# Kernel tuning notes

Hardware: AMD Instinct MI355X
Metric: run time of the kernel (lower is better)

Reference implementation:

```python
import jax, jax.numpy as jnp
import numpy as np

B, IN, HID, OUT = 1024, 512, 128, 64
INP1 = IN + 1  # 513, after prepending ones column


def setup_inputs() -> dict:
    key = jax.random.key(0)
    k1, k2, k3, k4, k5, k6, k7, k8 = jax.random.split(key, 8)
    s1 = 1.0 / np.sqrt(INP1 * INP1)
    s2 = 1.0 / np.sqrt(HID)
    return {
        "img": jax.random.normal(k1, (B, IN), dtype=jnp.float32),
        "tab": jax.random.normal(k2, (B, IN), dtype=jnp.float32),
        "W1": jax.random.uniform(k3, (HID, INP1 * INP1), jnp.float32, -s1, s1),
        "b1": jax.random.uniform(k4, (HID,), jnp.float32, -s1, s1),
        "W2": jax.random.uniform(k5, (HID, HID), jnp.float32, -s2, s2),
        "b2": jax.random.uniform(k6, (HID,), jnp.float32, -s2, s2),
        "W3": jax.random.uniform(k7, (OUT, HID), jnp.float32, -s2, s2),
        "b3": jax.random.uniform(k8, (OUT,), jnp.float32, -s2, s2),
    }


def reference(img, tab, W1, b1, W2, b2, W3, b3):
    ones = jnp.ones((img.shape[0], 1), dtype=img.dtype)
    x = jnp.concatenate([ones, img], axis=1)  # [B, IN+1]
    t = jnp.concatenate([ones, tab], axis=1)  # [B, IN+1]
    # batched outer product, flattened: [B, (IN+1)*(IN+1)]
    fusion = jnp.einsum("bi,bj->bij", x, t).reshape(x.shape[0], -1)
    # dropout is identity in eval mode
    y1 = fusion @ W1.T + b1
    y2 = jnp.tanh(y1 @ W2.T + b2)
    y3 = jax.nn.relu(y2 @ W3.T + b3)
    return y3
```

## Files before the change

kernel.cpp:

```cpp
#include <hip/hip_runtime.h>
#include <hip/hip_bf16.h>

typedef __bf16 bf16x8 __attribute__((ext_vector_type(8)));
typedef float f32x4 __attribute__((ext_vector_type(4)));
typedef float f32x4u __attribute__((ext_vector_type(4), aligned(4)));
typedef unsigned short u16x8 __attribute__((ext_vector_type(8)));

typedef __attribute__((address_space(1))) const unsigned int gu32;
typedef __attribute__((address_space(3))) unsigned int lu32;

#define B_SZ   1024
#define IN_SZ  512
#define HID    128
#define OUT_SZ 64
#define BK     32
#define NKT    16
#define M2     65536

static __device__ __forceinline__ unsigned short f2bf(float f) {
    __hip_bfloat16 h = __float2bfloat16(f);
    return *reinterpret_cast<unsigned short*>(&h);
}

__global__ __launch_bounds__(256) void prep_kernel(
    const float* __restrict__ img, const float* __restrict__ tab,
    const float* __restrict__ w1,
    unsigned short* __restrict__ tbt, float* __restrict__ xhT,
    float* __restrict__ tc, float* __restrict__ wrowT,
    unsigned short* __restrict__ w1c)
{
    const int blk = blockIdx.x;
    {
        const size_t e = ((size_t)blk * 256 + threadIdx.x) * 8;
        const int r  = (int)(e >> 9);
        const int c8 = (int)(e & 511);
        const size_t srow = (size_t)(r >> 9) * 513 + (r & 511);
        const float* src = w1 + srow * 513 + c8;
        const f32x4u lo = *reinterpret_cast<const f32x4u*>(src);
        const f32x4u hi = *reinterpret_cast<const f32x4u*>(src + 4);
        u16x8 u;
        u[0] = f2bf(lo[0]); u[1] = f2bf(lo[1]); u[2] = f2bf(lo[2]); u[3] = f2bf(lo[3]);
        u[4] = f2bf(hi[0]); u[5] = f2bf(hi[1]); u[6] = f2bf(hi[2]); u[7] = f2bf(hi[3]);
        *reinterpret_cast<u16x8*>(w1c + (size_t)r * 512 + c8) = u;
    }
    if (blk < 1024) {
        for (int j = threadIdx.x; j < 512; j += 256) {
            float v = (j == 0) ? 1.0f : tab[(size_t)blk * IN_SZ + (j - 1)];
            tbt[(size_t)blk * 512 + j] = f2bf(v);
        }
        if (threadIdx.x == 0) tc[blk] = tab[(size_t)blk * IN_SZ + 511];
    }
    if (blk < 513) {
        for (int b = threadIdx.x; b < B_SZ; b += 256)
            xhT[(size_t)blk * B_SZ + b] =
                (blk == 0) ? 1.0f : img[(size_t)b * IN_SZ + (blk - 1)];
    }
    if (blk < 257) {
        const int idx = blk * 256 + threadIdx.x;
        if (idx < 513 * 128) {
            const int j = idx >> 7, h = idx & 127;
            wrowT[idx] = w1[((size_t)h * 513 + 512) * 513 + j];
        }
    }
}

__global__ __launch_bounds__(256, 3) void gemm_fused(
    const float* __restrict__ w1, const unsigned short* __restrict__ w1c,
    const unsigned short* __restrict__ tbt,
    const float* __restrict__ xhT, const float* __restrict__ tc,
    float* __restrict__ y1acc)
{
    __shared__ unsigned short Als[3][128 * BK];
    __shared__ unsigned short Bls[3][128 * BK];

    const int wgid = (blockIdx.x & 7) * 512 + (blockIdx.x >> 3);
    const int bm = wgid >> 3;
    const int bn = wgid & 7;
    const int m0 = bm * 128;
    const int n0 = bn * 128;
    const int h0    = bm >> 2;
    const int ibase = (bm & 3) * 128;
    const int tid  = threadIdx.x;
    const int wv   = tid >> 6;
    const int wr   = wv >> 1;
    const int wc   = wv & 1;
    const int lane = tid & 63;
    const int l15  = lane & 15;
    const int kg   = lane >> 4;

    const unsigned short* asrc[2];
    const unsigned short* bsrc[2];
    int sBase[2];
    #pragma unroll
    for (int q = 0; q < 2; ++q) {
        const int p  = q * 256 + tid;
        const int r  = p >> 2;
        const int cl = (p & 3) ^ ((r >> 1) & 3);
        asrc[q] = w1c + (size_t)(m0 + r) * 512 + cl * 8;
        bsrc[q] = tbt + (size_t)(n0 + r) * 512 + cl * 8;
        sBase[q] = (q * 256 + wv * 64) * 8;
    }

    int aoffs[4], boffs[4];
    #pragma unroll
    for (int ms = 0; ms < 4; ++ms) {
        const int r = wr * 64 + ms * 16 + l15;
        aoffs[ms] = (r * 4 + (kg ^ ((r >> 1) & 3))) * 8;
    }
    #pragma unroll
    for (int ns = 0; ns < 4; ++ns) {
        const int r = wc * 64 + ns * 16 + l15;
        boffs[ns] = (r * 4 + (kg ^ ((r >> 1) & 3))) * 8;
    }

    f32x4 acc[4][4] = {};

#define STG(BUF, KT) do {                                                    \
        const int k32_ = (KT) * BK;                                          \
        _Pragma("unroll")                                                    \
        for (int q_ = 0; q_ < 2; ++q_) {                                     \
            __builtin_amdgcn_global_load_lds(                                \
                (gu32*)(const void*)(asrc[q_] + k32_),                       \
                (lu32*)(void*)&Als[BUF][sBase[q_]], 16, 0, 0);               \
            __builtin_amdgcn_global_load_lds(                                \
                (gu32*)(const void*)(bsrc[q_] + k32_),                       \
                (lu32*)(void*)&Bls[BUF][sBase[q_]], 16, 0, 0);               \
        }                                                                    \
    } while (0)

    STG(0, 0);
    STG(1, 1);

    #pragma unroll
    for (int kt = 0; kt < NKT; ++kt) {
        if (kt == NKT - 1) asm volatile("s_waitcnt vmcnt(0)" ::: "memory");
        else               asm volatile("s_waitcnt vmcnt(4)" ::: "memory");
        __builtin_amdgcn_s_barrier();
        __builtin_amdgcn_sched_barrier(0);

        if (kt + 2 < NKT) STG((kt + 2) % 3, kt + 2);

        const int cur = kt % 3;
        const unsigned short* ab = &Als[cur][0];
        const unsigned short* bb = &Bls[cur][0];
        bf16x8 af[4], bfr[4];
        #pragma unroll
        for (int ms = 0; ms < 4; ++ms)
            af[ms] = *reinterpret_cast<const bf16x8*>(&ab[aoffs[ms]]);
        #pragma unroll
        for (int ns = 0; ns < 4; ++ns)
            bfr[ns] = *reinterpret_cast<const bf16x8*>(&bb[boffs[ns]]);
        __builtin_amdgcn_s_setprio(1);
        #pragma unroll
        for (int ms = 0; ms < 4; ++ms)
            #pragma unroll
            for (int ns = 0; ns < 4; ++ns)
                acc[ms][ns] = __builtin_amdgcn_mfma_f32_16x16x32_bf16(
                    af[ms], bfr[ns], acc[ms][ns], 0, 0, 0);
        __builtin_amdgcn_s_setprio(0);
    }
#undef STG

    const size_t orow = (size_t)h0 * 513;
    float wcv[4][4];
    #pragma unroll
    for (int ms = 0; ms < 4; ++ms)
        #pragma unroll
        for (int v = 0; v < 4; ++v) {
            const int i_ = ibase + wr * 64 + ms * 16 + kg * 4 + v;
            wcv[ms][v] = w1[(orow + i_) * 513 + 512];
        }

    #pragma unroll
    for (int ns = 0; ns < 4; ++ns) {
        const int ncol = n0 + wc * 64 + ns * 16 + l15;
        const float tv = tc[ncol];
        float s0 = 0.f;
        #pragma unroll
        for (int ms = 0; ms < 4; ++ms) {
            const int i_ = ibase + wr * 64 + ms * 16 + kg * 4;
            #pragma unroll
            for (int v = 0; v < 4; ++v)
                s0 += (acc[ms][ns][v] + wcv[ms][v] * tv)
                      * xhT[(size_t)(i_ + v) * B_SZ + ncol];
        }
        s0 += __shfl_xor(s0, 16); s0 += __shfl_xor(s0, 32);
        if (lane < 16) atomicAdd(&y1acc[(size_t)ncol * HID + h0], s0);
    }
}

__global__ __launch_bounds__(128) void tailmlp_kernel(
    const float* __restrict__ img, const float* __restrict__ tab,
    const float* __restrict__ wrowT, const float* __restrict__ y1acc,
    const float* __restrict__ b1,
    const float* __restrict__ W2, const float* __restrict__ b2,
    const float* __restrict__ W3, const float* __restrict__ b3,
    float* __restrict__ out)
{
    __shared__ float tls[4][513];
    __shared__ float W2p[128][129];
    __shared__ float W3p[64][129];
    __shared__ float y1ls[4][128];
    __shared__ float y2ls[4][128];

    const int b0 = blockIdx.x * 4;
    const int h  = threadIdx.x;

    #pragma unroll
    for (int g = 0; g < 128; ++g) {
        const int idx = g * 128 + h;
        W2p[idx >> 7][idx & 127] = W2[idx];
    }
    #pragma unroll
    for (int g = 0; g < 64; ++g) {
        const int idx = g * 128 + h;
        W3p[idx >> 7][idx & 127] = W3[idx];
    }
    #pragma unroll
    for (int q = 0; q < 4; ++q)
        for (int j = h; j < 513; j += 128)
            tls[q][j] = (j == 0) ? 1.0f : tab[(size_t)(b0 + q) * IN_SZ + (j - 1)];
    __syncthreads();

    {
        float a0 = 0.f, a1 = 0.f, a2 = 0.f, a3 = 0.f;
        #pragma unroll 8
        for (int j = 0; j < 513; ++j) {
            const float w = wrowT[j * 128 + h];
            a0 += w * tls[0][j]; a1 += w * tls[1][j];
            a2 += w * tls[2][j]; a3 += w * tls[3][j];
        }
        const float bb = b1[h];
        y1ls[0][h] = y1acc[(size_t)(b0 + 0) * HID + h] + bb
                     + a0 * img[(size_t)(b0 + 0) * IN_SZ + 511];
        y1ls[1][h] = y1acc[(size_t)(b0 + 1) * HID + h] + bb
                     + a1 * img[(size_t)(b0 + 1) * IN_SZ + 511];
        y1ls[2][h] = y1acc[(size_t)(b0 + 2) * HID + h] + bb
                     + a2 * img[(size_t)(b0 + 2) * IN_SZ + 511];
        y1ls[3][h] = y1acc[(size_t)(b0 + 3) * HID + h] + bb
                     + a3 * img[(size_t)(b0 + 3) * IN_SZ + 511];
    }
    __syncthreads();

    {
        const float bb = b2[h];
        float s[4] = {bb, bb, bb, bb};
        #pragma unroll 16
        for (int k = 0; k < HID; ++k) {
            const float w = W2p[h][k];
            s[0] += w * y1ls[0][k]; s[1] += w * y1ls[1][k];
            s[2] += w * y1ls[2][k]; s[3] += w * y1ls[3][k];
        }
        #pragma unroll
        for (int q = 0; q < 4; ++q) y2ls[q][h] = tanhf(s[q]);
    }
    __syncthreads();

    if (h < OUT_SZ) {
        const float bb = b3[h];
        float s[4] = {bb, bb, bb, bb};
        #pragma unroll 16
        for (int k = 0; k < HID; ++k) {
            const float w = W3p[h][k];
            s[0] += w * y2ls[0][k]; s[1] += w * y2ls[1][k];
            s[2] += w * y2ls[2][k]; s[3] += w * y2ls[3][k];
        }
        #pragma unroll
        for (int q = 0; q < 4; ++q)
            out[(size_t)(b0 + q) * OUT_SZ + h] = fmaxf(s[q], 0.f);
    }
}

__global__ __launch_bounds__(512, 4) void gemm_fused_fb(
    const float* __restrict__ w1, const unsigned short* __restrict__ tbt,
    const float* __restrict__ xhT, const float* __restrict__ tc,
    float* __restrict__ y1acc)
{
    __shared__ float          Afs[2][64 * BK];
    __shared__ unsigned short Bls[2][512 * BK];

    const int bm = blockIdx.x >> 1;
    const int bn = blockIdx.x & 1;
    const int m0 = bm * 64;
    const int n0 = bn * 512;
    const int tid  = threadIdx.x;
    const int wv   = tid >> 6;
    const int lane = tid & 63;
    const int l15  = lane & 15;
    const int kg   = lane >> 4;

    const int ar  = tid >> 3;
    const int acl = (tid & 7) ^ (ar & 7);
    const float* asrc = w1 + (size_t)(m0 + ar) * 513 + acl * 4;
    const int aBase = (wv * 64) * 4;

    const unsigned short* bsrc[4];
    int bBase[4];
    #pragma unroll
    for (int q = 0; q < 4; ++q) {
        const int p  = q * 512 + tid;
        const int r  = p >> 2;
        const int cl = (p & 3) ^ ((r >> 1) & 3);
        bsrc[q] = tbt + (size_t)(n0 + r) * 512 + cl * 8;
        bBase[q] = (q * 512 + wv * 64) * 8;
    }

    int aoff0[4], aoff1[4], boffs[4];
    #pragma unroll
    for (int ms = 0; ms < 4; ++ms) {
        const int r = ms * 16 + l15;
        aoff0[ms] = r * 32 + (((kg * 2) + 0) ^ (r & 7)) * 4;
        aoff1[ms] = r * 32 + (((kg * 2) + 1) ^ (r & 7)) * 4;
    }
    #pragma unroll
    for (int ns = 0; ns < 4; ++ns) {
        const int r = wv * 64 + ns * 16 + l15;
        boffs[ns] = ((r << 2) | (kg ^ ((r >> 1) & 3))) * 8;
    }

    f32x4 acc[4][4] = {};

#define STAGE_FB(BUF, KT) do {                                               \
        const int k32_ = (KT) * BK;                                          \
        _Pragma("unroll")                                                    \
        for (int q_ = 0; q_ < 4; ++q_)                                       \
            __builtin_amdgcn_global_load_lds(                                \
                (gu32*)(const void*)(bsrc[q_] + k32_),                       \
                (lu32*)(void*)&Bls[BUF][bBase[q_]], 16, 0, 0);               \
        __builtin_amdgcn_global_load_lds(                                    \
            (gu32*)(const void*)(asrc + k32_),                               \
            (lu32*)(void*)&Afs[BUF][aBase], 16, 0, 0);                       \
    } while (0)

    STAGE_FB(0, 0);
    __syncthreads();

    for (int kt = 0; kt < NKT; ++kt) {
        const int cur = kt & 1;
        if (kt + 1 < NKT) STAGE_FB(cur ^ 1, kt + 1);

        const float*          ab = &Afs[cur][0];
        const unsigned short* bb = &Bls[cur][0];
        bf16x8 bfr[4];
        #pragma unroll
        for (int ns = 0; ns < 4; ++ns)
            bfr[ns] = *reinterpret_cast<const bf16x8*>(&bb[boffs[ns]]);
        #pragma unroll
        for (int ms = 0; ms < 4; ++ms) {
            const f32x4 lo = *reinterpret_cast<const f32x4*>(&ab[aoff0[ms]]);
            const f32x4 hi = *reinterpret_cast<const f32x4*>(&ab[aoff1[ms]]);
            u16x8 u;
            u[0] = f2bf(lo[0]); u[1] = f2bf(lo[1]);
            u[2] = f2bf(lo[2]); u[3] = f2bf(lo[3]);
            u[4] = f2bf(hi[0]); u[5] = f2bf(hi[1]);
            u[6] = f2bf(hi[2]); u[7] = f2bf(hi[3]);
            const bf16x8 af = __builtin_bit_cast(bf16x8, u);
            #pragma unroll
            for (int ns = 0; ns < 4; ++ns)
                acc[ms][ns] = __builtin_amdgcn_mfma_f32_16x16x32_bf16(
                    af, bfr[ns], acc[ms][ns], 0, 0, 0);
        }
        __syncthreads();
    }
#undef STAGE_FB

    const int h0 = m0 / 513;
    const int mb = (h0 + 1) * 513;
    const bool cross = (mb < m0 + 64);

    float wcv[4][4];
    #pragma unroll
    for (int ms = 0; ms < 4; ++ms)
        #pragma unroll
        for (int v = 0; v < 4; ++v)
            wcv[ms][v] = w1[(size_t)(m0 + ms * 16 + kg * 4 + v) * 513 + 512];

    #pragma unroll
    for (int ns = 0; ns < 4; ++ns) {
        const int ncol = n0 + wv * 64 + ns * 16 + l15;
        const float tv = tc[ncol];
        float s0 = 0.f, s1 = 0.f;
        #pragma unroll
        for (int ms = 0; ms < 4; ++ms) {
            #pragma unroll
            for (int v = 0; v < 4; ++v) {
                const int m = m0 + ms * 16 + kg * 4 + v;
                const bool lo = (m < mb);
                const int i = lo ? (m - h0 * 513) : (m - mb);
                const float val = (acc[ms][ns][v] + wcv[ms][v] * tv)
                                  * xhT[(size_t)i * B_SZ + ncol];
                if (lo) s0 += val; else s1 += val;
            }
        }
        s0 += __shfl_xor(s0, 16); s0 += __shfl_xor(s0, 32);
        if (lane < 16) atomicAdd(&y1acc[(size_t)ncol * HID + h0], s0);
        if (cross) {
            s1 += __shfl_xor(s1, 16); s1 += __shfl_xor(s1, 32);
            if (lane < 16 && (h0 + 1) < HID)
                atomicAdd(&y1acc[(size_t)ncol * HID + h0 + 1], s1);
        }
    }
}

__global__ __launch_bounds__(256) void prep_fb_kernel(
    const float* __restrict__ img, const float* __restrict__ tab,
    unsigned short* __restrict__ tbt, float* __restrict__ xhT,
    float* __restrict__ tc)
{
    const int blk = blockIdx.x;
    for (int j = threadIdx.x; j < 512; j += 256) {
        float v = (j == 0) ? 1.0f : tab[(size_t)blk * IN_SZ + (j - 1)];
        tbt[(size_t)blk * 512 + j] = f2bf(v);
    }
    if (threadIdx.x == 0) tc[blk] = tab[(size_t)blk * IN_SZ + 511];
    if (blk < 513) {
        for (int b = threadIdx.x; b < B_SZ; b += 256)
            xhT[(size_t)blk * B_SZ + b] =
                (blk == 0) ? 1.0f : img[(size_t)b * IN_SZ + (blk - 1)];
    }
}

__global__ __launch_bounds__(128) void mlp_kernel(
    const float* __restrict__ y1acc, const float* __restrict__ b1,
    const float* __restrict__ W2, const float* __restrict__ b2,
    const float* __restrict__ W3, const float* __restrict__ b3,
    float* __restrict__ out)
{
    __shared__ float y1r[HID];
    __shared__ float y2r[HID];
    const int b = blockIdx.x;
    const int h = threadIdx.x;
    y1r[h] = y1acc[(size_t)b * HID + h] + b1[h];
    __syncthreads();
    float a = b2[h];
    const float* w2r = W2 + (size_t)h * HID;
    #pragma unroll 8
    for (int k = 0; k < HID; ++k) a += w2r[k] * y1r[k];
    y2r[h] = tanhf(a);
    __syncthreads();
    if (h < OUT_SZ) {
        float a3 = b3[h];
        const float* w3r = W3 + (size_t)h * HID;
        #pragma unroll 8
        for (int k = 0; k < HID; ++k) a3 += w3r[k] * y2r[k];
        out[(size_t)b * OUT_SZ + h] = fmaxf(a3, 0.f);
    }
}

extern "C" void kernel_launch(void* const* d_in, const int* in_sizes, int n_in,
                              void* d_out, int out_size, void* d_ws, size_t ws_size,
                              hipStream_t stream) {
    const float* img = (const float*)d_in[0];
    const float* tab = (const float*)d_in[1];
    const float* W1  = (const float*)d_in[2];
    const float* b1  = (const float*)d_in[3];
    const float* W2  = (const float*)d_in[4];
    const float* b2  = (const float*)d_in[5];
    const float* W3  = (const float*)d_in[6];
    const float* b3  = (const float*)d_in[7];
    float* out = (float*)d_out;

    char* ws = (char*)d_ws;
    float*          y1acc = (float*)ws;
    unsigned short* tbt   = (unsigned short*)(ws + 524288);
    float*          xhT   = (float*)(ws + 1572864);
    float*          tc    = (float*)(ws + 3674112);
    float*          wrowT = (float*)(ws + 3678208);
    unsigned short* w1c   = (unsigned short*)(ws + 3940864);
    const size_t need = 3940864ULL + 67108864ULL;

    hipMemsetAsync(y1acc, 0, (size_t)B_SZ * HID * sizeof(float), stream);
    if (ws_size >= need) {
        prep_kernel<<<dim3(16384), dim3(256), 0, stream>>>(
            img, tab, W1, tbt, xhT, tc, wrowT, w1c);
        gemm_fused<<<dim3(4096), dim3(256), 0, stream>>>(
            W1, w1c, tbt, xhT, tc, y1acc);
        tailmlp_kernel<<<dim3(256), dim3(128), 0, stream>>>(
            img, tab, wrowT, y1acc, b1, W2, b2, W3, b3, out);
    } else {
        prep_fb_kernel<<<dim3(1024), dim3(256), 0, stream>>>(img, tab, tbt, xhT, tc);
        gemm_fused_fb<<<dim3(2052), dim3(512), 0, stream>>>(W1, tbt, xhT, tc, y1acc);
        mlp_kernel<<<dim3(1024), dim3(128), 0, stream>>>(y1acc, b1, W2, b2, W3, b3, out);
    }
}
```

Baseline: 199.1 us.

## Widen GEMM N-tile to 256 and split W1 repack into its own kernel

The fused GEMM now uses 128x256 output tiles per workgroup, each wave computing 4x8 MFMA tiles, so the grid shrinks from 4096 to 2048 blocks and each A tile from the large bf16 W1 copy is reused twice as much. The intent is to cut how often W1 is read from memory, at the cost of more accumulator registers (occupancy hint lowered from 3 to 2) and more LDS. The W1 fp32-to-bf16 repack moves from the combined prep kernel into a separate 512-thread kernel, and the small tab/img prep becomes a 1024-block kernel, which adds one extra launch.

Measured after the change: 198.8 us. No clear change (-0.2%).

```diff
diff --git a/kernel.cpp b/kernel.cpp
--- a/kernel.cpp
+++ b/kernel.cpp
@@ -22,34 +22,18 @@
     return *reinterpret_cast<unsigned short*>(&h);
 }
 
-__global__ __launch_bounds__(256) void prep_kernel(
+__global__ __launch_bounds__(256) void prep_small_kernel(
     const float* __restrict__ img, const float* __restrict__ tab,
-    const float* __restrict__ w1,
     unsigned short* __restrict__ tbt, float* __restrict__ xhT,
-    float* __restrict__ tc, float* __restrict__ wrowT,
-    unsigned short* __restrict__ w1c)
+    float* __restrict__ tc, const float* __restrict__ w1,
+    float* __restrict__ wrowT)
 {
     const int blk = blockIdx.x;
-    {
-        const size_t e = ((size_t)blk * 256 + threadIdx.x) * 8;
-        const int r  = (int)(e >> 9);
-        const int c8 = (int)(e & 511);
-        const size_t srow = (size_t)(r >> 9) * 513 + (r & 511);
-        const float* src = w1 + srow * 513 + c8;
-        const f32x4u lo = *reinterpret_cast<const f32x4u*>(src);
-        const f32x4u hi = *reinterpret_cast<const f32x4u*>(src + 4);
-        u16x8 u;
-        u[0] = f2bf(lo[0]); u[1] = f2bf(lo[1]); u[2] = f2bf(lo[2]); u[3] = f2bf(lo[3]);
-        u[4] = f2bf(hi[0]); u[5] = f2bf(hi[1]); u[6] = f2bf(hi[2]); u[7] = f2bf(hi[3]);
-        *reinterpret_cast<u16x8*>(w1c + (size_t)r * 512 + c8) = u;
-    }
-    if (blk < 1024) {
-        for (int j = threadIdx.x; j < 512; j += 256) {
-            float v = (j == 0) ? 1.0f : tab[(size_t)blk * IN_SZ + (j - 1)];
-            tbt[(size_t)blk * 512 + j] = f2bf(v);
-        }
-        if (threadIdx.x == 0) tc[blk] = tab[(size_t)blk * IN_SZ + 511];
-    }
+    for (int j = threadIdx.x; j < 512; j += 256) {
+        float v = (j == 0) ? 1.0f : tab[(size_t)blk * IN_SZ + (j - 1)];
+        tbt[(size_t)blk * 512 + j] = f2bf(v);
+    }
+    if (threadIdx.x == 0) tc[blk] = tab[(size_t)blk * IN_SZ + 511];
     if (blk < 513) {
         for (int b = threadIdx.x; b < B_SZ; b += 256)
             xhT[(size_t)blk * B_SZ + b] =
@@ -64,20 +48,36 @@
     }
 }
 
-__global__ __launch_bounds__(256, 3) void gemm_fused(
+__global__ __launch_bounds__(512) void repack_kernel(
+    const float* __restrict__ w1, unsigned short* __restrict__ w1c)
+{
+    const size_t e = ((size_t)blockIdx.x * 512 + threadIdx.x) * 8;
+    const int r  = (int)(e >> 9);
+    const int c8 = (int)(e & 511);
+    const size_t srow = (size_t)(r >> 9) * 513 + (r & 511);
+    const float* src = w1 + srow * 513 + c8;
+    const f32x4u lo = *reinterpret_cast<const f32x4u*>(src);
+    const f32x4u hi = *reinterpret_cast<const f32x4u*>(src + 4);
+    u16x8 u;
+    u[0] = f2bf(lo[0]); u[1] = f2bf(lo[1]); u[2] = f2bf(lo[2]); u[3] = f2bf(lo[3]);
+    u[4] = f2bf(hi[0]); u[5] = f2bf(hi[1]); u[6] = f2bf(hi[2]); u[7] = f2bf(hi[3]);
+    *reinterpret_cast<u16x8*>(w1c + (size_t)r * 512 + c8) = u;
+}
+
+__global__ __launch_bounds__(256, 2) void gemm_fused(
     const float* __restrict__ w1, const unsigned short* __restrict__ w1c,
     const unsigned short* __restrict__ tbt,
     const float* __restrict__ xhT, const float* __restrict__ tc,
     float* __restrict__ y1acc)
 {
     __shared__ unsigned short Als[3][128 * BK];
-    __shared__ unsigned short Bls[3][128 * BK];
-
-    const int wgid = (blockIdx.x & 7) * 512 + (blockIdx.x >> 3);
-    const int bm = wgid >> 3;
-    const int bn = wgid & 7;
+    __shared__ unsigned short Bls[3][256 * BK];
+
+    const int wgid = (blockIdx.x & 7) * 256 + (blockIdx.x >> 3);
+    const int bm = wgid >> 2;
+    const int bn = wgid & 3;
     const int m0 = bm * 128;
-    const int n0 = bn * 128;
+    const int n0 = bn * 256;
     const int h0    = bm >> 2;
     const int ibase = (bm & 3) * 128;
     const int tid  = threadIdx.x;
@@ -89,43 +89,52 @@
     const int kg   = lane >> 4;
 
     const unsigned short* asrc[2];
-    const unsigned short* bsrc[2];
-    int sBase[2];
+    int aBase[2];
     #pragma unroll
     for (int q = 0; q < 2; ++q) {
         const int p  = q * 256 + tid;
         const int r  = p >> 2;
         const int cl = (p & 3) ^ ((r >> 1) & 3);
         asrc[q] = w1c + (size_t)(m0 + r) * 512 + cl * 8;
+        aBase[q] = (q * 256 + wv * 64) * 8;
+    }
+    const unsigned short* bsrc[4];
+    int bBase[4];
+    #pragma unroll
+    for (int q = 0; q < 4; ++q) {
+        const int p  = q * 256 + tid;
+        const int r  = p >> 2;
+        const int cl = (p & 3) ^ ((r >> 1) & 3);
         bsrc[q] = tbt + (size_t)(n0 + r) * 512 + cl * 8;
-        sBase[q] = (q * 256 + wv * 64) * 8;
-    }
-
-    int aoffs[4], boffs[4];
+        bBase[q] = (q * 256 + wv * 64) * 8;
+    }
+
+    int aoffs[4], boffs[8];
     #pragma unroll
     for (int ms = 0; ms < 4; ++ms) {
         const int r = wr * 64 + ms * 16 + l15;
         aoffs[ms] = (r * 4 + (kg ^ ((r >> 1) & 3))) * 8;
     }
     #pragma unroll
-    for (int ns = 0; ns < 4; ++ns) {
-        const int r = wc * 64 + ns * 16 + l15;
+    for (int ns = 0; ns < 8; ++ns) {
+        const int r = wc * 128 + ns * 16 + l15;
         boffs[ns] = (r * 4 + (kg ^ ((r >> 1) & 3))) * 8;
     }
 
-    f32x4 acc[4][4] = {};
+    f32x4 acc[4][8] = {};
 
 #define STG(BUF, KT) do {                                                    \
         const int k32_ = (KT) * BK;                                          \
         _Pragma("unroll")                                                    \
-        for (int q_ = 0; q_ < 2; ++q_) {                                     \
+        for (int q_ = 0; q_ < 2; ++q_)                                       \
             __builtin_amdgcn_global_load_lds(                                \
                 (gu32*)(const void*)(asrc[q_] + k32_),                       \
-                (lu32*)(void*)&Als[BUF][sBase[q_]], 16, 0, 0);               \
+                (lu32*)(void*)&Als[BUF][aBase[q_]], 16, 0, 0);               \
+        _Pragma("unroll")                                                    \
+        for (int q_ = 0; q_ < 4; ++q_)                                       \
             __builtin_amdgcn_global_load_lds(                                \
                 (gu32*)(const void*)(bsrc[q_] + k32_),                       \
-                (lu32*)(void*)&Bls[BUF][sBase[q_]], 16, 0, 0);               \
-        }                                                                    \
+                (lu32*)(void*)&Bls[BUF][bBase[q_]], 16, 0, 0);               \
     } while (0)
 
     STG(0, 0);
@@ -134,7 +143,7 @@
     #pragma unroll
     for (int kt = 0; kt < NKT; ++kt) {
         if (kt == NKT - 1) asm volatile("s_waitcnt vmcnt(0)" ::: "memory");
-        else               asm volatile("s_waitcnt vmcnt(4)" ::: "memory");
+        else               asm volatile("s_waitcnt vmcnt(6)" ::: "memory");
         __builtin_amdgcn_s_barrier();
         __builtin_amdgcn_sched_barrier(0);
 
@@ -143,18 +152,18 @@
         const int cur = kt % 3;
         const unsigned short* ab = &Als[cur][0];
         const unsigned short* bb = &Bls[cur][0];
-        bf16x8 af[4], bfr[4];
+        bf16x8 af[4], bfr[8];
         #pragma unroll
         for (int ms = 0; ms < 4; ++ms)
             af[ms] = *reinterpret_cast<const bf16x8*>(&ab[aoffs[ms]]);
         #pragma unroll
-        for (int ns = 0; ns < 4; ++ns)
+        for (int ns = 0; ns < 8; ++ns)
             bfr[ns] = *reinterpret_cast<const bf16x8*>(&bb[boffs[ns]]);
         __builtin_amdgcn_s_setprio(1);
         #pragma unroll
         for (int ms = 0; ms < 4; ++ms)
             #pragma unroll
-            for (int ns = 0; ns < 4; ++ns)
+            for (int ns = 0; ns < 8; ++ns)
                 acc[ms][ns] = __builtin_amdgcn_mfma_f32_16x16x32_bf16(
                     af[ms], bfr[ns], acc[ms][ns], 0, 0, 0);
         __builtin_amdgcn_s_setprio(0);
@@ -172,8 +181,8 @@
         }
 
     #pragma unroll
-    for (int ns = 0; ns < 4; ++ns) {
-        const int ncol = n0 + wc * 64 + ns * 16 + l15;
+    for (int ns = 0; ns < 8; ++ns) {
+        const int ncol = n0 + wc * 128 + ns * 16 + l15;
         const float tv = tc[ncol];
         float s0 = 0.f;
         #pragma unroll
@@ -471,9 +480,10 @@
 
     hipMemsetAsync(y1acc, 0, (size_t)B_SZ * HID * sizeof(float), stream);
     if (ws_size >= need) {
-        prep_kernel<<<dim3(16384), dim3(256), 0, stream>>>(
-            img, tab, W1, tbt, xhT, tc, wrowT, w1c);
-        gemm_fused<<<dim3(4096), dim3(256), 0, stream>>>(
+        prep_small_kernel<<<dim3(1024), dim3(256), 0, stream>>>(
+            img, tab, tbt, xhT, tc, W1, wrowT);
+        repack_kernel<<<dim3(8192), dim3(512), 0, stream>>>(W1, w1c);
+        gemm_fused<<<dim3(2048), dim3(256), 0, stream>>>(
             W1, w1c, tbt, xhT, tc, y1acc);
         tailmlp_kernel<<<dim3(256), dim3(128), 0, stream>>>(
             img, tab, wrowT, y1acc, b1, W2, b2, W3, b3, out);
```

## Fuse W1 bf16 conversion into first GEMM column block, split GEMM into two kernels

Applied to the files above, without the earlier changes.

The separate fp32-to-bf16 conversion pass over W1 is removed from the prep kernel. A new GEMM kernel (512 workgroups, 512 threads, 128x256 tiles) handles the first 256 batch columns while reading fp32 W1 directly. It converts each tile in registers, feeds it to LDS for the MFMA and writes the bf16 copy to the workspace. The remaining 768 columns run in the existing bf16 GEMM kernel, which reads that cached copy. This saves one full read pass over the 128 MB fp32 W1, but adds a kernel boundary and a less parallel first stage.

Result: no change. 198.0 us (-0.6%).

```diff
diff --git a/kernel.cpp b/kernel.cpp
--- a/kernel.cpp
+++ b/kernel.cpp
@@ -21,35 +21,25 @@
     __hip_bfloat16 h = __float2bfloat16(f);
     return *reinterpret_cast<unsigned short*>(&h);
 }
-
-__global__ __launch_bounds__(256) void prep_kernel(
+static __device__ __forceinline__ u16x8 cv8(f32x4u lo, f32x4u hi) {
+    u16x8 u;
+    u[0] = f2bf(lo[0]); u[1] = f2bf(lo[1]); u[2] = f2bf(lo[2]); u[3] = f2bf(lo[3]);
+    u[4] = f2bf(hi[0]); u[5] = f2bf(hi[1]); u[6] = f2bf(hi[2]); u[7] = f2bf(hi[3]);
+    return u;
+}
+
+__global__ __launch_bounds__(256) void prep_small_kernel(
     const float* __restrict__ img, const float* __restrict__ tab,
-    const float* __restrict__ w1,
     unsigned short* __restrict__ tbt, float* __restrict__ xhT,
-    float* __restrict__ tc, float* __restrict__ wrowT,
-    unsigned short* __restrict__ w1c)
+    float* __restrict__ tc, const float* __restrict__ w1,
+    float* __restrict__ wrowT)
 {
     const int blk = blockIdx.x;
-    {
-        const size_t e = ((size_t)blk * 256 + threadIdx.x) * 8;
-        const int r  = (int)(e >> 9);
-        const int c8 = (int)(e & 511);
-        const size_t srow = (size_t)(r >> 9) * 513 + (r & 511);
-        const float* src = w1 + srow * 513 + c8;
-        const f32x4u lo = *reinterpret_cast<const f32x4u*>(src);
-        const f32x4u hi = *reinterpret_cast<const f32x4u*>(src + 4);
-        u16x8 u;
-        u[0] = f2bf(lo[0]); u[1] = f2bf(lo[1]); u[2] = f2bf(lo[2]); u[3] = f2bf(lo[3]);
-        u[4] = f2bf(hi[0]); u[5] = f2bf(hi[1]); u[6] = f2bf(hi[2]); u[7] = f2bf(hi[3]);
-        *reinterpret_cast<u16x8*>(w1c + (size_t)r * 512 + c8) = u;
-    }
-    if (blk < 1024) {
-        for (int j = threadIdx.x; j < 512; j += 256) {
-            float v = (j == 0) ? 1.0f : tab[(size_t)blk * IN_SZ + (j - 1)];
-            tbt[(size_t)blk * 512 + j] = f2bf(v);
-        }
-        if (threadIdx.x == 0) tc[blk] = tab[(size_t)blk * IN_SZ + 511];
-    }
+    for (int j = threadIdx.x; j < 512; j += 256) {
+        float v = (j == 0) ? 1.0f : tab[(size_t)blk * IN_SZ + (j - 1)];
+        tbt[(size_t)blk * 512 + j] = f2bf(v);
+    }
+    if (threadIdx.x == 0) tc[blk] = tab[(size_t)blk * IN_SZ + 511];
     if (blk < 513) {
         for (int b = threadIdx.x; b < B_SZ; b += 256)
             xhT[(size_t)blk * B_SZ + b] =
@@ -64,7 +54,155 @@
     }
 }
 
-__global__ __launch_bounds__(256, 3) void gemm_fused(
+__global__ __launch_bounds__(512, 4) void gemm_r(
+    const float* __restrict__ w1, const unsigned short* __restrict__ tbt,
+    const float* __restrict__ xhT, const float* __restrict__ tc,
+    float* __restrict__ y1acc, unsigned short* __restrict__ w1c)
+{
+    __shared__ unsigned short Als[3][128 * BK];
+    __shared__ unsigned short Bls[3][256 * BK];
+
+    const int wgid = (blockIdx.x & 7) * 64 + (blockIdx.x >> 3);
+    const int bm = wgid;
+    const int n0 = 0;
+    const int h0    = bm >> 2;
+    const int ibase = (bm & 3) * 128;
+    const int tid  = threadIdx.x;
+    const int wv   = tid >> 6;
+    const int wr   = wv >> 2;
+    const int wc   = wv & 3;
+    const int lane = tid & 63;
+    const int l15  = lane & 15;
+    const int kg   = lane >> 4;
+
+    const int ar  = tid >> 2;
+    const int acl = (tid & 3) ^ ((ar >> 1) & 3);
+    const float* asrcF = w1 + ((size_t)h0 * 513 + ibase + ar) * 513 + acl * 8;
+    unsigned short* wdst = w1c + ((size_t)bm * 128 + ar) * 512 + acl * 8;
+
+    const unsigned short* bsrc[2];
+    int bBase[2];
+    #pragma unroll
+    for (int q = 0; q < 2; ++q) {
+        const int p  = q * 512 + tid;
+        const int r  = p >> 2;
+        const int cl = (p & 3) ^ ((r >> 1) & 3);
+        bsrc[q] = tbt + (size_t)(n0 + r) * 512 + cl * 8;
+        bBase[q] = (q * 512 + wv * 64) * 8;
+    }
+
+    int aoffs[4], boffs[4];
+    #pragma unroll
+    for (int ms = 0; ms < 4; ++ms) {
+        const int r = wr * 64 + ms * 16 + l15;
+        aoffs[ms] = (r * 4 + (kg ^ ((r >> 1) & 3))) * 8;
+    }
+    #pragma unroll
+    for (int ns = 0; ns < 4; ++ns) {
+        const int r = wc * 64 + ns * 16 + l15;
+        boffs[ns] = (r * 4 + (kg ^ ((r >> 1) & 3))) * 8;
+    }
+
+    f32x4 acc[4][4] = {};
+    f32x4u rAlo, rAhi;
+
+#define STB(BUF, KT) do {                                                    \
+        const int k32_ = (KT) * BK;                                          \
+        _Pragma("unroll")                                                    \
+        for (int q_ = 0; q_ < 2; ++q_)                                       \
+            __builtin_amdgcn_global_load_lds(                                \
+                (gu32*)(const void*)(bsrc[q_] + k32_),                       \
+                (lu32*)(void*)&Bls[BUF][bBase[q_]], 16, 0, 0);               \
+    } while (0)
+
+    {
+        const f32x4u t0lo = *reinterpret_cast<const f32x4u*>(asrcF);
+        const f32x4u t0hi = *reinterpret_cast<const f32x4u*>(asrcF + 4);
+        const f32x4u t1lo = *reinterpret_cast<const f32x4u*>(asrcF + 32);
+        const f32x4u t1hi = *reinterpret_cast<const f32x4u*>(asrcF + 36);
+        const u16x8 u0 = cv8(t0lo, t0hi);
+        const u16x8 u1 = cv8(t1lo, t1hi);
+        *reinterpret_cast<u16x8*>(&Als[0][tid * 8]) = u0;
+        *reinterpret_cast<u16x8*>(&Als[1][tid * 8]) = u1;
+        *reinterpret_cast<u16x8*>(wdst + 0 * BK) = u0;
+        *reinterpret_cast<u16x8*>(wdst + 1 * BK) = u1;
+        STB(0, 0);
+        STB(1, 1);
+    }
+    __syncthreads();
+
+    #pragma unroll
+    for (int kt = 0; kt < NKT; ++kt) {
+        const int cur = kt % 3;
+        const unsigned short* ab = &Als[cur][0];
+        const unsigned short* bb = &Bls[cur][0];
+
+        if (kt >= 1 && kt + 1 < NKT) {
+            const u16x8 u = cv8(rAlo, rAhi);
+            *reinterpret_cast<u16x8*>(&Als[(kt + 1) % 3][tid * 8]) = u;
+            *reinterpret_cast<u16x8*>(wdst + (kt + 1) * BK) = u;
+        }
+        if (kt + 2 < NKT) {
+            const float* s_ = asrcF + (kt + 2) * 32;
+            rAlo = *reinterpret_cast<const f32x4u*>(s_);
+            rAhi = *reinterpret_cast<const f32x4u*>(s_ + 4);
+        }
+
+        bf16x8 af[4];
+        #pragma unroll
+        for (int ms = 0; ms < 4; ++ms)
+            af[ms] = *reinterpret_cast<const bf16x8*>(&ab[aoffs[ms]]);
+        __builtin_amdgcn_s_setprio(1);
+        #pragma unroll
+        for (int ns = 0; ns < 4; ++ns) {
+            const bf16x8 bf = *reinterpret_cast<const bf16x8*>(&bb[boffs[ns]]);
+            #pragma unroll
+            for (int ms = 0; ms < 4; ++ms)
+                acc[ms][ns] = __builtin_amdgcn_mfma_f32_16x16x32_bf16(
+                    af[ms], bf, acc[ms][ns], 0, 0, 0);
+        }
+        __builtin_amdgcn_s_setprio(0);
+
+        if (kt == NKT - 1) break;
+
+        if (kt + 2 >= NKT) asm volatile("s_waitcnt vmcnt(0)" ::: "memory");
+        else               asm volatile("s_waitcnt vmcnt(2)" ::: "memory");
+        if (kt + 2 < NKT) STB((kt + 2) % 3, kt + 2);
+        asm volatile("s_waitcnt lgkmcnt(0)" ::: "memory");
+        __builtin_amdgcn_s_barrier();
+        __builtin_amdgcn_sched_barrier(0);
+    }
+#undef STB
+
+    const size_t orow = (size_t)h0 * 513;
+    float wcv[4][4];
+    #pragma unroll
+    for (int ms = 0; ms < 4; ++ms)
+        #pragma unroll
+        for (int v = 0; v < 4; ++v) {
+            const int i_ = ibase + wr * 64 + ms * 16 + kg * 4 + v;
+            wcv[ms][v] = w1[(orow + i_) * 513 + 512];
+        }
+
+    #pragma unroll
+    for (int ns = 0; ns < 4; ++ns) {
+        const int ncol = n0 + wc * 64 + ns * 16 + l15;
+        const float tv = tc[ncol];
+        float s0 = 0.f;
+        #pragma unroll
+        for (int ms = 0; ms < 4; ++ms) {
+            const int i_ = ibase + wr * 64 + ms * 16 + kg * 4;
+            #pragma unroll
+            for (int v = 0; v < 4; ++v)
+                s0 += (acc[ms][ns][v] + wcv[ms][v] * tv)
+                      * xhT[(size_t)(i_ + v) * B_SZ + ncol];
+        }
+        s0 += __shfl_xor(s0, 16); s0 += __shfl_xor(s0, 32);
+        if (lane < 16) atomicAdd(&y1acc[(size_t)ncol * HID + h0], s0);
+    }
+}
+
+__global__ __launch_bounds__(256, 3) void gemm_g(
     const float* __restrict__ w1, const unsigned short* __restrict__ w1c,
     const unsigned short* __restrict__ tbt,
     const float* __restrict__ xhT, const float* __restrict__ tc,
@@ -73,11 +211,11 @@
     __shared__ unsigned short Als[3][128 * BK];
     __shared__ unsigned short Bls[3][128 * BK];
 
-    const int wgid = (blockIdx.x & 7) * 512 + (blockIdx.x >> 3);
-    const int bm = wgid >> 3;
-    const int bn = wgid & 7;
+    const int wgid = (blockIdx.x & 7) * 384 + (blockIdx.x >> 3);
+    const int bm = wgid / 6;
+    const int bn = wgid % 6;
     const int m0 = bm * 128;
-    const int n0 = bn * 128;
+    const int n0 = 256 + bn * 128;
     const int h0    = bm >> 2;
     const int ibase = (bm & 3) * 128;
     const int tid  = threadIdx.x;
@@ -471,9 +609,11 @@
 
     hipMemsetAsync(y1acc, 0, (size_t)B_SZ * HID * sizeof(float), stream);
     if (ws_size >= need) {
-        prep_kernel<<<dim3(16384), dim3(256), 0, stream>>>(
-            img, tab, W1, tbt, xhT, tc, wrowT, w1c);
-        gemm_fused<<<dim3(4096), dim3(256), 0, stream>>>(
+        prep_small_kernel<<<dim3(1024), dim3(256), 0, stream>>>(
+            img, tab, tbt, xhT, tc, W1, wrowT);
+        gemm_r<<<dim3(512), dim3(512), 0, stream>>>(
+            W1, tbt, xhT, tc, y1acc, w1c);
+        gemm_g<<<dim3(3072), dim3(256), 0, stream>>>(
             W1, w1c, tbt, xhT, tc, y1acc);
         tailmlp_kernel<<<dim3(256), dim3(128), 0, stream>>>(
             img, tab, wrowT, y1acc, b1, W2, b2, W3, b3, out);
```
